# Performance work log

Hardware: AMD Instinct MI355X
Metric: run time of the kernel (lower is better)

The kernel has to match this reference:

```python
import jax, jax.numpy as jnp
import numpy as np

QW_MAX = 127  # 2**(8-1) - 1


def setup_inputs() -> dict:
    key = jax.random.key(0)
    k1, k2, k3, k4, k5 = jax.random.split(key, 5)
    B, Din, H, Dout = 4096, 1024, 4096, 1024
    x = jax.random.normal(k1, (B, Din), dtype=jnp.float32)
    # float master weights (already transposed, as in quantify_weights: weight.T)
    w1f = jax.random.normal(k2, (Din, H), dtype=jnp.float32) * 0.02
    b1f = jax.random.normal(k3, (H,), dtype=jnp.float32) * 0.02
    w2f = jax.random.normal(k4, (H, Dout), dtype=jnp.float32) * 0.02
    b2f = jax.random.normal(k5, (Dout,), dtype=jnp.float32) * 0.02
    return {"x": x, "w1f": w1f, "b1f": b1f, "w2f": w2f, "b2f": b2f}


def _quantify_pair(w, b):
    # joint max-abs scale over weight and bias (matches quantify(x, x2))
    max_v = jnp.maximum(jnp.max(jnp.abs(w)), jnp.max(jnp.abs(b)))
    scale = max_v / QW_MAX
    wq = jnp.round(w / scale).astype(jnp.int8)
    bq = jnp.round(b / scale).astype(jnp.int8)
    return wq, bq, scale


def _dot_product(q_a, q_b, scale_a, scale_b, target_scale):
    # int8 GEMM with int32 accumulation, then requantize to int16
    y0 = q_a.astype(jnp.int32) @ q_b.astype(jnp.int32)  # [M, N] int32
    scale = scale_a * scale_b / target_scale
    return jnp.round(y0 * scale).astype(jnp.int16)


def reference(x, w1f, b1f, w2f, b2f):
    # weight quantization (done once at init in torch, inlined here)
    w1, b1, s1 = _quantify_pair(w1f, b1f)
    w2, b2, s2 = _quantify_pair(w2f, b2f)
    # dynamic activation quantization
    x_scale = jnp.max(jnp.abs(x)) / QW_MAX
    x_q = jnp.round(x / x_scale).astype(jnp.int8)
    # layer 1: target_scale = s1, so effective multiplier is x_scale
    o1 = _dot_product(x_q, w1, x_scale, s1, s1) + b1.astype(jnp.int16)
    # layer 2: note torch passes scale_1 (not x_scale) here — faithful to source
    o2 = _dot_product(jnp.maximum(o1, 0), w2, s1, s2, s2) + b2.astype(jnp.int16)
    # dequantize
    return o2.astype(jnp.float32) * s2
```

## Files before the change

kernel.cpp:

```cpp
#include <hip/hip_runtime.h>
#include <stdint.h>

typedef int   i32x4 __attribute__((ext_vector_type(4)));
typedef float f32x4 __attribute__((ext_vector_type(4)));

#define WS_PART    0
#define WS_XQ      32768
#define WS_W1QT    (WS_XQ   + 4096*1024)
#define WS_W2QT    (WS_W1QT + 4096*1024)
#define WS_PS      (WS_W2QT + 4096*1024)
#define WS_PH      (WS_PS   + 4096*4096)

__device__ __forceinline__ void async16(const void* g, void* l) {
  __builtin_amdgcn_global_load_lds(
      (const __attribute__((address_space(1))) unsigned*)g,
      (__attribute__((address_space(3))) unsigned*)l, 16, 0, 0);
}

__device__ __forceinline__ float block_absmax(const float* __restrict__ p0, int n0,
                                              const float* __restrict__ p1, int n1,
                                              float* red, float* slot) {
  int tid = threadIdx.x, nt = blockDim.x;
  float m = 0.f;
  for (int i = tid; i < n0; i += nt) m = fmaxf(m, fabsf(p0[i]));
  if (p1) for (int i = tid; i < n1; i += nt) m = fmaxf(m, fabsf(p1[i]));
  for (int off = 32; off; off >>= 1) m = fmaxf(m, __shfl_down(m, off));
  if ((tid & 63) == 0) red[tid >> 6] = m;
  __syncthreads();
  if (tid == 0) {
    int nw = nt >> 6;
    float M = red[0];
    for (int w = 1; w < nw; w++) M = fmaxf(M, red[w]);
    *slot = M;
  }
  __syncthreads();
  return *slot;
}

__global__ void k_absmax3(const float* __restrict__ x, const float* __restrict__ w1,
                          const float* __restrict__ w2, float* __restrict__ part) {
  int seg = blockIdx.x >> 9;
  int b = blockIdx.x & 511;
  const float* p = (seg == 0) ? x : (seg == 1) ? w1 : w2;
  int i = b * 256 + threadIdx.x;
  float m = 0.f;
  #pragma unroll
  for (int it = 0; it < 8; it++) {
    f32x4 v = ((const f32x4*)p)[i + it * 131072];
    m = fmaxf(m, fmaxf(fmaxf(fabsf(v.x), fabsf(v.y)), fmaxf(fabsf(v.z), fabsf(v.w))));
  }
  for (int off = 32; off; off >>= 1) m = fmaxf(m, __shfl_down(m, off));
  __shared__ float red[4];
  if ((threadIdx.x & 63) == 0) red[threadIdx.x >> 6] = m;
  __syncthreads();
  if (threadIdx.x == 0)
    part[blockIdx.x] = fmaxf(fmaxf(red[0], red[1]), fmaxf(red[2], red[3]));
}

__device__ __forceinline__ void quantT_body(const float* __restrict__ w, float s,
                                            i32x4* __restrict__ out, int C, int tkbits,
                                            int b) {
  int L = b * 256 + threadIdx.x;
  int h_in = L & 127;
  int kb = (L >> 7) & 3;
  int tk = (L >> 9) & ((1 << tkbits) - 1);
  int hblk = L >> (9 + tkbits);
  int h = hblk * 128 + h_in;
  int k0 = (tk * 4 + kb) * 16;
  int wd[4];
  #pragma unroll
  for (int d = 0; d < 4; d++) {
    unsigned acc = 0;
    #pragma unroll
    for (int j = 0; j < 4; j++) {
      float v = w[(size_t)(k0 + d * 4 + j) * C + h];
      int q = (int)rintf(v / s) & 255;
      acc |= (unsigned)q << (8 * j);
    }
    wd[d] = (int)acc;
  }
  i32x4 o; o.x = wd[0]; o.y = wd[1]; o.z = wd[2]; o.w = wd[3];
  out[L] = o;
}

__global__ void k_prep(const float* __restrict__ x, const float* __restrict__ w1f,
                       const float* __restrict__ w2f, const float* __restrict__ b1f,
                       const float* __restrict__ b2f, const float* __restrict__ part,
                       i32x4* __restrict__ xq, i32x4* __restrict__ w1qt,
                       i32x4* __restrict__ w2qt) {
  __shared__ float red[4];
  __shared__ float slot;
  int seg = blockIdx.x >> 10;
  int b = blockIdx.x & 1023;
  if (seg == 0) {
    float s = block_absmax(part, 512, nullptr, 0, red, &slot) / 127.0f;
    int L = b * 256 + threadIdx.x;
    int m_in = L & 127, kb = (L >> 7) & 3, tk = (L >> 9) & 15, mblk = L >> 13;
    int m = mblk * 128 + m_in;
    int k0 = (tk * 4 + kb) * 16;
    const f32x4* px = (const f32x4*)(x + m * 1024 + k0);
    int wd[4];
    #pragma unroll
    for (int d = 0; d < 4; d++) {
      f32x4 v = px[d];
      int b0 = (int)rintf(v.x / s) & 255;
      int b1 = (int)rintf(v.y / s) & 255;
      int b2 = (int)rintf(v.z / s) & 255;
      int b3 = (int)rintf(v.w / s) & 255;
      wd[d] = b0 | (b1 << 8) | (b2 << 16) | (b3 << 24);
    }
    i32x4 o; o.x = wd[0]; o.y = wd[1]; o.z = wd[2]; o.w = wd[3];
    xq[L] = o;
  } else if (seg == 1) {
    float s = block_absmax(part + 512, 512, b1f, 4096, red, &slot) / 127.0f;
    quantT_body(w1f, s, w1qt, 4096, 4, b);
  } else {
    float s = block_absmax(part + 1024, 512, b2f, 1024, red, &slot) / 127.0f;
    quantT_body(w2f, s, w2qt, 1024, 6, b);
  }
}

__launch_bounds__(256, 4)
__global__ void k_gemm1(const i32x4* __restrict__ Aq, const i32x4* __restrict__ Bq,
                        const float* __restrict__ part, const float* __restrict__ b1f,
                        unsigned* __restrict__ plane_s, unsigned* __restrict__ plane_h) {
  __shared__ i32x4 As[2][512];
  __shared__ float red[4];
  __shared__ float slot;
  __shared__ int b1s[128];
  int tid = threadIdx.x;
  int bb = blockIdx.x;
  int hb = blockIdx.y;
  int lane = tid & 63, wid = tid >> 6;
  int wm = wid & 1, wn = wid >> 1;
  int g = lane >> 4, l15 = lane & 15;

  const i32x4* gA = Aq + (size_t)hb * 16 * 512;
  const i32x4* gB = Bq + (size_t)bb * 16 * 512;

  int abase = g * 128 + wm * 64 + l15;
  int bbase = g * 128 + wn * 64 + l15;

  async16(gA + tid, &As[0][tid]);
  async16(gA + tid + 256, &As[0][tid + 256]);
  i32x4 bnow[4];
  #pragma unroll
  for (int c = 0; c < 4; c++) bnow[c] = gB[bbase + c * 16];

  float sx  = block_absmax(part, 512, nullptr, 0, red, &slot) / 127.0f;
  float s1v = block_absmax(part + 512, 512, b1f, 4096, red, &slot) / 127.0f;
  float mult1 = sx * s1v / s1v;
  for (int i = tid; i < 128; i += 256)
    b1s[i] = (int)rintf(b1f[hb * 128 + i] / s1v);

  i32x4 acc[4][4];
  #pragma unroll
  for (int r = 0; r < 4; r++)
    #pragma unroll
    for (int c = 0; c < 4; c++) acc[r][c] = (i32x4)(0);

  for (int t = 0; t < 16; ++t) {
    int cur = t & 1;
    if (t + 1 < 16) {
      const i32x4* ga = gA + (t + 1) * 512;
      async16(ga + tid, &As[cur ^ 1][tid]);
      async16(ga + tid + 256, &As[cur ^ 1][tid + 256]);
    }
    i32x4 af[4];
    #pragma unroll
    for (int r = 0; r < 4; r++) af[r] = As[cur][abase + r * 16];
    #pragma unroll
    for (int r = 0; r < 4; r++)
      #pragma unroll
      for (int c = 0; c < 4; c++)
        acc[r][c] = __builtin_amdgcn_mfma_i32_16x16x64_i8(af[r], bnow[c], acc[r][c], 0, 0, 0);
    if (t + 1 < 16) {
      const i32x4* gb = gB + (t + 1) * 512;
      #pragma unroll
      for (int c = 0; c < 4; c++) bnow[c] = gb[bbase + c * 16];
    }
    __syncthreads();
  }

  int t2base = hb * 2 + wm;
  #pragma unroll
  for (int r = 0; r < 4; r++) {
    int hloc = wm * 64 + r * 16 + 4 * g;
    int bq0 = b1s[hloc], bq1 = b1s[hloc + 1], bq2 = b1s[hloc + 2], bq3 = b1s[hloc + 3];
    #pragma unroll
    for (int c = 0; c < 4; c++) {
      unsigned lo = 0, hi = 0;
      #pragma unroll
      for (int q = 0; q < 4; q++) {
        int y0 = acc[r][c][q];
        int bqv = (q == 0) ? bq0 : (q == 1) ? bq1 : (q == 2) ? bq2 : bq3;
        int o = (short)((int)rintf((float)y0 * mult1) + bqv);
        int a = o > 0 ? o : 0;
        int s8 = (int)(signed char)(a & 0xFF);
        int h8 = (a >> 8) + (s8 < 0 ? 1 : 0);
        lo |= (unsigned)(s8 & 0xFF) << (8 * q);
        hi |= (unsigned)(h8 & 0xFF) << (8 * q);
      }
      int m_in = wn * 64 + c * 16 + l15;
      unsigned idx = (((unsigned)(bb * 64 + t2base) * 512u + (unsigned)(r * 128 + m_in)) << 2) + g;
      plane_s[idx] = lo;
      plane_h[idx] = hi;
    }
  }
}

__launch_bounds__(512, 4)
__global__ void k_gemm2(const i32x4* __restrict__ Ps, const i32x4* __restrict__ Ph,
                        const i32x4* __restrict__ Bq, const float* __restrict__ part,
                        const float* __restrict__ b1f, const float* __restrict__ b2f,
                        float* __restrict__ out) {
  __shared__ i32x4 st[2048];
  __shared__ float red[8];
  __shared__ float slot;

  int tid = threadIdx.x;
  int L = blockIdx.x;
  int mb = ((L & 7) << 3) | ((L >> 3) & 7);
  int nb = L >> 6;
  int mblk = mb >> 1, half = mb & 1;
  int wid = tid >> 6, lane = tid & 63;
  int kh = wid >> 2, w2 = wid & 3;
  int wm = w2 & 1, wn = w2 >> 1;
  int g = lane >> 4, l15 = lane & 15;
  int t256 = tid & 255;
  int khbase = kh * 1024;
  int a_idx = (t256 >> 6) * 128 + half * 64 + (t256 & 63);
  int abase = g * 64 + wm * 32 + l15;
  int bbase = g * 128 + wn * 64 + l15;

  const i32x4* gS = Ps + (((size_t)mblk * 64 + kh * 32) << 9);
  const i32x4* gH = Ph + (((size_t)mblk * 64 + kh * 32) << 9);
  const i32x4* gB = Bq + (((size_t)nb * 64 + kh * 32) << 9);

  async16(gS + a_idx, &st[khbase + t256]);
  async16(gH + a_idx, &st[khbase + 256 + t256]);
  i32x4 bnow[4];
  #pragma unroll
  for (int c = 0; c < 4; c++) bnow[c] = gB[bbase + c * 16];

  float s1v = block_absmax(part + 512, 512, b1f, 4096, red, &slot) / 127.0f;
  float s2v = block_absmax(part + 1024, 512, b2f, 1024, red, &slot) / 127.0f;
  float mult2 = s1v * s2v / s2v;
  int bq[4];
  #pragma unroll
  for (int c = 0; c < 4; c++)
    bq[c] = (int)rintf(b2f[nb * 128 + wn * 64 + c * 16 + l15] / s2v);

  i32x4 accS[2][4], accH[2][4];
  #pragma unroll
  for (int r = 0; r < 2; r++)
    #pragma unroll
    for (int c = 0; c < 4; c++) { accS[r][c] = (i32x4)(0); accH[r][c] = (i32x4)(0); }

  for (int tt = 0; tt < 32; ++tt) {
    int cur = tt & 1;
    if (tt + 1 < 32) {
      const i32x4* pS = gS + ((size_t)(tt + 1) << 9);
      const i32x4* pH = gH + ((size_t)(tt + 1) << 9);
      int R1 = khbase + (cur ^ 1) * 512;
      async16(pS + a_idx, &st[R1 + t256]);
      async16(pH + a_idx, &st[R1 + 256 + t256]);
    }
    int R = khbase + cur * 512;
    i32x4 aS[2], aH[2];
    #pragma unroll
    for (int r = 0; r < 2; r++) {
      aS[r] = st[R + abase + r * 16];
      aH[r] = st[R + 256 + abase + r * 16];
    }
    #pragma unroll
    for (int r = 0; r < 2; r++)
      #pragma unroll
      for (int c = 0; c < 4; c++) {
        accS[r][c] = __builtin_amdgcn_mfma_i32_16x16x64_i8(aS[r], bnow[c], accS[r][c], 0, 0, 0);
        accH[r][c] = __builtin_amdgcn_mfma_i32_16x16x64_i8(aH[r], bnow[c], accH[r][c], 0, 0, 0);
      }
    if (tt + 1 < 32) {
      const i32x4* pB = gB + ((size_t)(tt + 1) << 9);
      #pragma unroll
      for (int c = 0; c < 4; c++) bnow[c] = pB[bbase + c * 16];
    }
    __syncthreads();
  }

  int* mg = (int*)st;
  if (kh == 1) {
    #pragma unroll
    for (int r = 0; r < 2; r++)
      #pragma unroll
      for (int c = 0; c < 4; c++)
        #pragma unroll
        for (int q = 0; q < 4; q++)
          mg[((r * 4 + c) * 4 + q) * 256 + t256] = accS[r][c][q] + accH[r][c][q] * 256;
  }
  __syncthreads();
  if (kh == 0) {
    #pragma unroll
    for (int r = 0; r < 2; r++) {
      int m0 = mb * 64 + wm * 32 + r * 16 + 4 * g;
      #pragma unroll
      for (int c = 0; c < 4; c++) {
        int n = nb * 128 + wn * 64 + c * 16 + l15;
        #pragma unroll
        for (int q = 0; q < 4; q++) {
          int y0 = accS[r][c][q] + accH[r][c][q] * 256
                 + mg[((r * 4 + c) * 4 + q) * 256 + t256];
          int o = (short)((int)rintf((float)y0 * mult2) + bq[c]);
          out[(size_t)(m0 + q) * 1024 + n] = (float)o * s2v;
        }
      }
    }
  }
}

extern "C" void kernel_launch(void* const* d_in, const int* in_sizes, int n_in,
                              void* d_out, int out_size, void* d_ws, size_t ws_size,
                              hipStream_t stream) {
  const float* x   = (const float*)d_in[0];
  const float* w1f = (const float*)d_in[1];
  const float* b1f = (const float*)d_in[2];
  const float* w2f = (const float*)d_in[3];
  const float* b2f = (const float*)d_in[4];
  float* out = (float*)d_out;

  char* ws = (char*)d_ws;
  float*  part    = (float*)(ws + WS_PART);
  i32x4*  xq      = (i32x4*)(ws + WS_XQ);
  i32x4*  w1qt    = (i32x4*)(ws + WS_W1QT);
  i32x4*  w2qt    = (i32x4*)(ws + WS_W2QT);
  unsigned* ps    = (unsigned*)(ws + WS_PS);
  unsigned* ph    = (unsigned*)(ws + WS_PH);

  k_absmax3<<<1536, 256, 0, stream>>>(x, w1f, w2f, part);
  k_prep<<<3072, 256, 0, stream>>>(x, w1f, w2f, b1f, b2f, part, xq, w1qt, w2qt);
  k_gemm1<<<dim3(32, 32), 256, 0, stream>>>(w1qt, xq, part, b1f, ps, ph);
  k_gemm2<<<512, 512, 0, stream>>>((const i32x4*)ps, (const i32x4*)ph, w2qt,
                                   part, b1f, b2f, out);
}
```

Baseline: 186.7 us.

## Drop LDS staging in both int8 GEMMs and load fragments directly from global

Both GEMM kernels stop staging A tiles through shared memory with async global-to-LDS copies and per-iteration barriers. Each wave now loads its MFMA fragments straight from global into registers, with a one-step register prefetch. The second GEMM uses 32-row tiles and twice as many blocks, and its split-K merge uses a smaller LDS buffer. This removes LDS traffic and barriers but gives up intra-block reuse of A tiles, so L2/global load traffic per MFMA rises.

```diff
diff --git a/kernel.cpp b/kernel.cpp
--- a/kernel.cpp
+++ b/kernel.cpp
@@ -10,12 +10,6 @@
 #define WS_W2QT    (WS_W1QT + 4096*1024)
 #define WS_PS      (WS_W2QT + 4096*1024)
 #define WS_PH      (WS_PS   + 4096*4096)
-
-__device__ __forceinline__ void async16(const void* g, void* l) {
-  __builtin_amdgcn_global_load_lds(
-      (const __attribute__((address_space(1))) unsigned*)g,
-      (__attribute__((address_space(3))) unsigned*)l, 16, 0, 0);
-}
 
 __device__ __forceinline__ float block_absmax(const float* __restrict__ p0, int n0,
                                               const float* __restrict__ p1, int n1,
@@ -124,7 +118,6 @@
 __global__ void k_gemm1(const i32x4* __restrict__ Aq, const i32x4* __restrict__ Bq,
                         const float* __restrict__ part, const float* __restrict__ b1f,
                         unsigned* __restrict__ plane_s, unsigned* __restrict__ plane_h) {
-  __shared__ i32x4 As[2][512];
   __shared__ float red[4];
   __shared__ float slot;
   __shared__ int b1s[128];
@@ -135,23 +128,20 @@
   int wm = wid & 1, wn = wid >> 1;
   int g = lane >> 4, l15 = lane & 15;
 
-  const i32x4* gA = Aq + (size_t)hb * 16 * 512;
-  const i32x4* gB = Bq + (size_t)bb * 16 * 512;
-
-  int abase = g * 128 + wm * 64 + l15;
-  int bbase = g * 128 + wn * 64 + l15;
-
-  async16(gA + tid, &As[0][tid]);
-  async16(gA + tid + 256, &As[0][tid + 256]);
-  i32x4 bnow[4];
-  #pragma unroll
-  for (int c = 0; c < 4; c++) bnow[c] = gB[bbase + c * 16];
+  const i32x4* gA = Aq + (size_t)hb * 16 * 512 + g * 128 + wm * 64 + l15;
+  const i32x4* gB = Bq + (size_t)bb * 16 * 512 + g * 128 + wn * 64 + l15;
+
+  i32x4 af[4], bf[4];
+  #pragma unroll
+  for (int r = 0; r < 4; r++) af[r] = gA[r * 16];
+  #pragma unroll
+  for (int c = 0; c < 4; c++) bf[c] = gB[c * 16];
 
   float sx  = block_absmax(part, 512, nullptr, 0, red, &slot) / 127.0f;
   float s1v = block_absmax(part + 512, 512, b1f, 4096, red, &slot) / 127.0f;
   float mult1 = sx * s1v / s1v;
-  for (int i = tid; i < 128; i += 256)
-    b1s[i] = (int)rintf(b1f[hb * 128 + i] / s1v);
+  if (tid < 128) b1s[tid] = (int)rintf(b1f[hb * 128 + tid] / s1v);
+  __syncthreads();
 
   i32x4 acc[4][4];
   #pragma unroll
@@ -160,26 +150,18 @@
     for (int c = 0; c < 4; c++) acc[r][c] = (i32x4)(0);
 
   for (int t = 0; t < 16; ++t) {
-    int cur = t & 1;
-    if (t + 1 < 16) {
-      const i32x4* ga = gA + (t + 1) * 512;
-      async16(ga + tid, &As[cur ^ 1][tid]);
-      async16(ga + tid + 256, &As[cur ^ 1][tid + 256]);
-    }
-    i32x4 af[4];
-    #pragma unroll
-    for (int r = 0; r < 4; r++) af[r] = As[cur][abase + r * 16];
-    #pragma unroll
-    for (int r = 0; r < 4; r++)
+    int tn = (t + 1 < 16) ? (t + 1) : 15;
+    const i32x4* gAn = gA + (size_t)tn * 512;
+    const i32x4* gBn = gB + (size_t)tn * 512;
+    #pragma unroll
+    for (int r = 0; r < 4; r++) {
       #pragma unroll
       for (int c = 0; c < 4; c++)
-        acc[r][c] = __builtin_amdgcn_mfma_i32_16x16x64_i8(af[r], bnow[c], acc[r][c], 0, 0, 0);
-    if (t + 1 < 16) {
-      const i32x4* gb = gB + (t + 1) * 512;
-      #pragma unroll
-      for (int c = 0; c < 4; c++) bnow[c] = gb[bbase + c * 16];
-    }
-    __syncthreads();
+        acc[r][c] = __builtin_amdgcn_mfma_i32_16x16x64_i8(af[r], bf[c], acc[r][c], 0, 0, 0);
+      af[r] = gAn[r * 16];
+    }
+    #pragma unroll
+    for (int c = 0; c < 4; c++) bf[c] = gBn[c * 16];
   }
 
   int t2base = hb * 2 + wm;
@@ -214,34 +196,28 @@
                         const i32x4* __restrict__ Bq, const float* __restrict__ part,
                         const float* __restrict__ b1f, const float* __restrict__ b2f,
                         float* __restrict__ out) {
-  __shared__ i32x4 st[2048];
   __shared__ float red[8];
   __shared__ float slot;
-
+  __shared__ int mg[32 * 128];
   int tid = threadIdx.x;
   int L = blockIdx.x;
-  int mb = ((L & 7) << 3) | ((L >> 3) & 7);
-  int nb = L >> 6;
-  int mblk = mb >> 1, half = mb & 1;
+  int mb = L & 127;
+  int nb = L >> 7;
+  int mblk = mb >> 2;
+  int m128 = (mb & 3) * 32;
   int wid = tid >> 6, lane = tid & 63;
   int kh = wid >> 2, w2 = wid & 3;
   int wm = w2 & 1, wn = w2 >> 1;
   int g = lane >> 4, l15 = lane & 15;
-  int t256 = tid & 255;
-  int khbase = kh * 1024;
-  int a_idx = (t256 >> 6) * 128 + half * 64 + (t256 & 63);
-  int abase = g * 64 + wm * 32 + l15;
-  int bbase = g * 128 + wn * 64 + l15;
-
-  const i32x4* gS = Ps + (((size_t)mblk * 64 + kh * 32) << 9);
-  const i32x4* gH = Ph + (((size_t)mblk * 64 + kh * 32) << 9);
-  const i32x4* gB = Bq + (((size_t)nb * 64 + kh * 32) << 9);
-
-  async16(gS + a_idx, &st[khbase + t256]);
-  async16(gH + a_idx, &st[khbase + 256 + t256]);
-  i32x4 bnow[4];
-  #pragma unroll
-  for (int c = 0; c < 4; c++) bnow[c] = gB[bbase + c * 16];
+
+  const i32x4* gS = Ps + (((size_t)mblk * 64 + kh * 32) << 9) + g * 128 + m128 + wm * 16 + l15;
+  const i32x4* gH = Ph + (((size_t)mblk * 64 + kh * 32) << 9) + g * 128 + m128 + wm * 16 + l15;
+  const i32x4* gB = Bq + (((size_t)nb * 64 + kh * 32) << 9) + g * 128 + wn * 64 + l15;
+
+  i32x4 aS = gS[0], aH = gH[0];
+  i32x4 bf[4];
+  #pragma unroll
+  for (int c = 0; c < 4; c++) bf[c] = gB[c * 16];
 
   float s1v = block_absmax(part + 512, 512, b1f, 4096, red, &slot) / 127.0f;
   float s2v = block_absmax(part + 1024, 512, b2f, 1024, red, &slot) / 127.0f;
@@ -251,68 +227,49 @@
   for (int c = 0; c < 4; c++)
     bq[c] = (int)rintf(b2f[nb * 128 + wn * 64 + c * 16 + l15] / s2v);
 
-  i32x4 accS[2][4], accH[2][4];
-  #pragma unroll
-  for (int r = 0; r < 2; r++)
-    #pragma unroll
-    for (int c = 0; c < 4; c++) { accS[r][c] = (i32x4)(0); accH[r][c] = (i32x4)(0); }
-
+  i32x4 accS[4], accH[4];
+  #pragma unroll
+  for (int c = 0; c < 4; c++) { accS[c] = (i32x4)(0); accH[c] = (i32x4)(0); }
+
+  #pragma unroll 2
   for (int tt = 0; tt < 32; ++tt) {
-    int cur = tt & 1;
-    if (tt + 1 < 32) {
-      const i32x4* pS = gS + ((size_t)(tt + 1) << 9);
-      const i32x4* pH = gH + ((size_t)(tt + 1) << 9);
-      int R1 = khbase + (cur ^ 1) * 512;
-      async16(pS + a_idx, &st[R1 + t256]);
-      async16(pH + a_idx, &st[R1 + 256 + t256]);
-    }
-    int R = khbase + cur * 512;
-    i32x4 aS[2], aH[2];
-    #pragma unroll
-    for (int r = 0; r < 2; r++) {
-      aS[r] = st[R + abase + r * 16];
-      aH[r] = st[R + 256 + abase + r * 16];
-    }
-    #pragma unroll
-    for (int r = 0; r < 2; r++)
+    int tn = (tt + 1 < 32) ? (tt + 1) : 31;
+    const i32x4* pS = gS + (size_t)tn * 512;
+    const i32x4* pH = gH + (size_t)tn * 512;
+    const i32x4* pB = gB + (size_t)tn * 512;
+    i32x4 aSn = pS[0], aHn = pH[0];
+    i32x4 bn[4];
+    #pragma unroll
+    for (int c = 0; c < 4; c++) bn[c] = pB[c * 16];
+    #pragma unroll
+    for (int c = 0; c < 4; c++) {
+      accS[c] = __builtin_amdgcn_mfma_i32_16x16x64_i8(aS, bf[c], accS[c], 0, 0, 0);
+      accH[c] = __builtin_amdgcn_mfma_i32_16x16x64_i8(aH, bf[c], accH[c], 0, 0, 0);
+    }
+    aS = aSn; aH = aHn;
+    #pragma unroll
+    for (int c = 0; c < 4; c++) bf[c] = bn[c];
+  }
+
+  if (kh == 1) {
+    #pragma unroll
+    for (int c = 0; c < 4; c++)
       #pragma unroll
-      for (int c = 0; c < 4; c++) {
-        accS[r][c] = __builtin_amdgcn_mfma_i32_16x16x64_i8(aS[r], bnow[c], accS[r][c], 0, 0, 0);
-        accH[r][c] = __builtin_amdgcn_mfma_i32_16x16x64_i8(aH[r], bnow[c], accH[r][c], 0, 0, 0);
-      }
-    if (tt + 1 < 32) {
-      const i32x4* pB = gB + ((size_t)(tt + 1) << 9);
+      for (int q = 0; q < 4; q++)
+        mg[(wm * 16 + 4 * g + q) * 128 + wn * 64 + c * 16 + l15] =
+            accS[c][q] + accH[c][q] * 256;
+  }
+  __syncthreads();
+  if (kh == 0) {
+    #pragma unroll
+    for (int c = 0; c < 4; c++) {
+      int n = nb * 128 + wn * 64 + c * 16 + l15;
       #pragma unroll
-      for (int c = 0; c < 4; c++) bnow[c] = pB[bbase + c * 16];
-    }
-    __syncthreads();
-  }
-
-  int* mg = (int*)st;
-  if (kh == 1) {
-    #pragma unroll
-    for (int r = 0; r < 2; r++)
-      #pragma unroll
-      for (int c = 0; c < 4; c++)
-        #pragma unroll
-        for (int q = 0; q < 4; q++)
-          mg[((r * 4 + c) * 4 + q) * 256 + t256] = accS[r][c][q] + accH[r][c][q] * 256;
-  }
-  __syncthreads();
-  if (kh == 0) {
-    #pragma unroll
-    for (int r = 0; r < 2; r++) {
-      int m0 = mb * 64 + wm * 32 + r * 16 + 4 * g;
-      #pragma unroll
-      for (int c = 0; c < 4; c++) {
-        int n = nb * 128 + wn * 64 + c * 16 + l15;
-        #pragma unroll
-        for (int q = 0; q < 4; q++) {
-          int y0 = accS[r][c][q] + accH[r][c][q] * 256
-                 + mg[((r * 4 + c) * 4 + q) * 256 + t256];
-          int o = (short)((int)rintf((float)y0 * mult2) + bq[c]);
-          out[(size_t)(m0 + q) * 1024 + n] = (float)o * s2v;
-        }
+      for (int q = 0; q < 4; q++) {
+        int rloc = wm * 16 + 4 * g + q;
+        int y0 = accS[c][q] + accH[c][q] * 256 + mg[rloc * 128 + wn * 64 + c * 16 + l15];
+        int o = (short)((int)rintf((float)y0 * mult2) + bq[c]);
+        out[(size_t)(mb * 32 + rloc) * 1024 + n] = (float)o * s2v;
       }
     }
   }
@@ -339,6 +296,6 @@
   k_absmax3<<<1536, 256, 0, stream>>>(x, w1f, w2f, part);
   k_prep<<<3072, 256, 0, stream>>>(x, w1f, w2f, b1f, b2f, part, xq, w1qt, w2qt);
   k_gemm1<<<dim3(32, 32), 256, 0, stream>>>(w1qt, xq, part, b1f, ps, ph);
-  k_gemm2<<<512, 512, 0, stream>>>((const i32x4*)ps, (const i32x4*)ph, w2qt,
-                                   part, b1f, b2f, out);
-}
+  k_gemm2<<<1024, 512, 0, stream>>>((const i32x4*)ps, (const i32x4*)ph, w2qt,
+                                    part, b1f, b2f, out);
+}
```

New measurement: 204.3 us. 1.09x slower.

## Triple-buffer A and B tiles in LDS for both GEMMs, drop split-K in gemm2

Applied to the files above, without the earlier changes.

Both int8 GEMM kernels now stage A and B tiles through LDS with a three-deep async buffer ring, prefetching two K-steps ahead. Before, B fragments were loaded straight from global memory into registers, which exposed that latency on every step. gemm2 also drops its two-wave-group split-K and the LDS merge at the end, running 256 threads over all 64 K-steps. This removes the reduction pass, but each block now does a longer serial K loop with fewer waves. LDS use grows and launch bounds go down to 3 blocks per CU, which may lower occupancy.

```diff
diff --git a/kernel.cpp b/kernel.cpp
--- a/kernel.cpp
+++ b/kernel.cpp
@@ -120,11 +120,12 @@
   }
 }
 
-__launch_bounds__(256, 4)
+__launch_bounds__(256, 3)
 __global__ void k_gemm1(const i32x4* __restrict__ Aq, const i32x4* __restrict__ Bq,
                         const float* __restrict__ part, const float* __restrict__ b1f,
                         unsigned* __restrict__ plane_s, unsigned* __restrict__ plane_h) {
-  __shared__ i32x4 As[2][512];
+  __shared__ i32x4 As[3][512];
+  __shared__ i32x4 Bs[3][512];
   __shared__ float red[4];
   __shared__ float slot;
   __shared__ int b1s[128];
@@ -141,17 +142,20 @@
   int abase = g * 128 + wm * 64 + l15;
   int bbase = g * 128 + wn * 64 + l15;
 
-  async16(gA + tid, &As[0][tid]);
-  async16(gA + tid + 256, &As[0][tid + 256]);
-  i32x4 bnow[4];
-  #pragma unroll
-  for (int c = 0; c < 4; c++) bnow[c] = gB[bbase + c * 16];
+  #pragma unroll
+  for (int p = 0; p < 2; p++) {
+    const i32x4* ga = gA + p * 512;
+    const i32x4* gb = gB + p * 512;
+    async16(ga + tid, &As[p][tid]);
+    async16(ga + tid + 256, &As[p][tid + 256]);
+    async16(gb + tid, &Bs[p][tid]);
+    async16(gb + tid + 256, &Bs[p][tid + 256]);
+  }
 
   float sx  = block_absmax(part, 512, nullptr, 0, red, &slot) / 127.0f;
   float s1v = block_absmax(part + 512, 512, b1f, 4096, red, &slot) / 127.0f;
   float mult1 = sx * s1v / s1v;
-  for (int i = tid; i < 128; i += 256)
-    b1s[i] = (int)rintf(b1f[hb * 128 + i] / s1v);
+  if (tid < 128) b1s[tid] = (int)rintf(b1f[hb * 128 + tid] / s1v);
 
   i32x4 acc[4][4];
   #pragma unroll
@@ -159,27 +163,29 @@
     #pragma unroll
     for (int c = 0; c < 4; c++) acc[r][c] = (i32x4)(0);
 
+  int cur = 0, wr = 2;
   for (int t = 0; t < 16; ++t) {
-    int cur = t & 1;
-    if (t + 1 < 16) {
-      const i32x4* ga = gA + (t + 1) * 512;
-      async16(ga + tid, &As[cur ^ 1][tid]);
-      async16(ga + tid + 256, &As[cur ^ 1][tid + 256]);
-    }
-    i32x4 af[4];
+    __syncthreads();
+    if (t + 2 < 16) {
+      const i32x4* ga = gA + (t + 2) * 512;
+      const i32x4* gb = gB + (t + 2) * 512;
+      async16(ga + tid, &As[wr][tid]);
+      async16(ga + tid + 256, &As[wr][tid + 256]);
+      async16(gb + tid, &Bs[wr][tid]);
+      async16(gb + tid + 256, &Bs[wr][tid + 256]);
+    }
+    i32x4 af[4], bf[4];
     #pragma unroll
     for (int r = 0; r < 4; r++) af[r] = As[cur][abase + r * 16];
+    #pragma unroll
+    for (int c = 0; c < 4; c++) bf[c] = Bs[cur][bbase + c * 16];
     #pragma unroll
     for (int r = 0; r < 4; r++)
       #pragma unroll
       for (int c = 0; c < 4; c++)
-        acc[r][c] = __builtin_amdgcn_mfma_i32_16x16x64_i8(af[r], bnow[c], acc[r][c], 0, 0, 0);
-    if (t + 1 < 16) {
-      const i32x4* gb = gB + (t + 1) * 512;
-      #pragma unroll
-      for (int c = 0; c < 4; c++) bnow[c] = gb[bbase + c * 16];
-    }
-    __syncthreads();
+        acc[r][c] = __builtin_amdgcn_mfma_i32_16x16x64_i8(af[r], bf[c], acc[r][c], 0, 0, 0);
+    cur = (cur == 2) ? 0 : cur + 1;
+    wr  = (wr  == 2) ? 0 : wr  + 1;
   }
 
   int t2base = hb * 2 + wm;
@@ -209,39 +215,39 @@
   }
 }
 
-__launch_bounds__(512, 4)
+__launch_bounds__(256, 3)
 __global__ void k_gemm2(const i32x4* __restrict__ Ps, const i32x4* __restrict__ Ph,
                         const i32x4* __restrict__ Bq, const float* __restrict__ part,
                         const float* __restrict__ b1f, const float* __restrict__ b2f,
                         float* __restrict__ out) {
-  __shared__ i32x4 st[2048];
-  __shared__ float red[8];
+  __shared__ i32x4 sS[3][256];
+  __shared__ i32x4 sH[3][256];
+  __shared__ i32x4 sB[3][512];
+  __shared__ float red[4];
   __shared__ float slot;
-
   int tid = threadIdx.x;
   int L = blockIdx.x;
   int mb = ((L & 7) << 3) | ((L >> 3) & 7);
   int nb = L >> 6;
   int mblk = mb >> 1, half = mb & 1;
-  int wid = tid >> 6, lane = tid & 63;
-  int kh = wid >> 2, w2 = wid & 3;
-  int wm = w2 & 1, wn = w2 >> 1;
+  int lane = tid & 63, wid = tid >> 6;
+  int wm = wid & 1, wn = wid >> 1;
   int g = lane >> 4, l15 = lane & 15;
-  int t256 = tid & 255;
-  int khbase = kh * 1024;
-  int a_idx = (t256 >> 6) * 128 + half * 64 + (t256 & 63);
+  int a_idx = (tid >> 6) * 128 + half * 64 + (tid & 63);
   int abase = g * 64 + wm * 32 + l15;
   int bbase = g * 128 + wn * 64 + l15;
 
-  const i32x4* gS = Ps + (((size_t)mblk * 64 + kh * 32) << 9);
-  const i32x4* gH = Ph + (((size_t)mblk * 64 + kh * 32) << 9);
-  const i32x4* gB = Bq + (((size_t)nb * 64 + kh * 32) << 9);
-
-  async16(gS + a_idx, &st[khbase + t256]);
-  async16(gH + a_idx, &st[khbase + 256 + t256]);
-  i32x4 bnow[4];
-  #pragma unroll
-  for (int c = 0; c < 4; c++) bnow[c] = gB[bbase + c * 16];
+  const i32x4* gS = Ps + ((size_t)mblk * 64 << 9);
+  const i32x4* gH = Ph + ((size_t)mblk * 64 << 9);
+  const i32x4* gB = Bq + ((size_t)nb * 64 << 9);
+
+  #pragma unroll
+  for (int p = 0; p < 2; p++) {
+    async16(gS + p * 512 + a_idx, &sS[p][tid]);
+    async16(gH + p * 512 + a_idx, &sH[p][tid]);
+    async16(gB + p * 512 + tid, &sB[p][tid]);
+    async16(gB + p * 512 + tid + 256, &sB[p][tid + 256]);
+  }
 
   float s1v = block_absmax(part + 512, 512, b1f, 4096, red, &slot) / 127.0f;
   float s2v = block_absmax(part + 1024, 512, b2f, 1024, red, &slot) / 127.0f;
@@ -257,62 +263,49 @@
     #pragma unroll
     for (int c = 0; c < 4; c++) { accS[r][c] = (i32x4)(0); accH[r][c] = (i32x4)(0); }
 
-  for (int tt = 0; tt < 32; ++tt) {
-    int cur = tt & 1;
-    if (tt + 1 < 32) {
-      const i32x4* pS = gS + ((size_t)(tt + 1) << 9);
-      const i32x4* pH = gH + ((size_t)(tt + 1) << 9);
-      int R1 = khbase + (cur ^ 1) * 512;
-      async16(pS + a_idx, &st[R1 + t256]);
-      async16(pH + a_idx, &st[R1 + 256 + t256]);
-    }
-    int R = khbase + cur * 512;
-    i32x4 aS[2], aH[2];
+  int cur = 0, wr = 2;
+  for (int t = 0; t < 64; ++t) {
+    __syncthreads();
+    if (t + 2 < 64) {
+      const i32x4* pS = gS + (size_t)(t + 2) * 512;
+      const i32x4* pH = gH + (size_t)(t + 2) * 512;
+      const i32x4* pB = gB + (size_t)(t + 2) * 512;
+      async16(pS + a_idx, &sS[wr][tid]);
+      async16(pH + a_idx, &sH[wr][tid]);
+      async16(pB + tid, &sB[wr][tid]);
+      async16(pB + tid + 256, &sB[wr][tid + 256]);
+    }
+    i32x4 aS[2], aH[2], bf[4];
     #pragma unroll
     for (int r = 0; r < 2; r++) {
-      aS[r] = st[R + abase + r * 16];
-      aH[r] = st[R + 256 + abase + r * 16];
-    }
+      aS[r] = sS[cur][abase + r * 16];
+      aH[r] = sH[cur][abase + r * 16];
+    }
+    #pragma unroll
+    for (int c = 0; c < 4; c++) bf[c] = sB[cur][bbase + c * 16];
     #pragma unroll
     for (int r = 0; r < 2; r++)
       #pragma unroll
       for (int c = 0; c < 4; c++) {
-        accS[r][c] = __builtin_amdgcn_mfma_i32_16x16x64_i8(aS[r], bnow[c], accS[r][c], 0, 0, 0);
-        accH[r][c] = __builtin_amdgcn_mfma_i32_16x16x64_i8(aH[r], bnow[c], accH[r][c], 0, 0, 0);
+        accS[r][c] = __builtin_amdgcn_mfma_i32_16x16x64_i8(aS[r], bf[c], accS[r][c], 0, 0, 0);
+        accH[r][c] = __builtin_amdgcn_mfma_i32_16x16x64_i8(aH[r], bf[c], accH[r][c], 0, 0, 0);
       }
-    if (tt + 1 < 32) {
-      const i32x4* pB = gB + ((size_t)(tt + 1) << 9);
+    cur = (cur == 2) ? 0 : cur + 1;
+    wr  = (wr  == 2) ? 0 : wr  + 1;
+  }
+
+  float s2 = s2v;
+  #pragma unroll
+  for (int r = 0; r < 2; r++) {
+    int m0 = mb * 64 + wm * 32 + r * 16 + 4 * g;
+    #pragma unroll
+    for (int c = 0; c < 4; c++) {
+      int n = nb * 128 + wn * 64 + c * 16 + l15;
       #pragma unroll
-      for (int c = 0; c < 4; c++) bnow[c] = pB[bbase + c * 16];
-    }
-    __syncthreads();
-  }
-
-  int* mg = (int*)st;
-  if (kh == 1) {
-    #pragma unroll
-    for (int r = 0; r < 2; r++)
-      #pragma unroll
-      for (int c = 0; c < 4; c++)
-        #pragma unroll
-        for (int q = 0; q < 4; q++)
-          mg[((r * 4 + c) * 4 + q) * 256 + t256] = accS[r][c][q] + accH[r][c][q] * 256;
-  }
-  __syncthreads();
-  if (kh == 0) {
-    #pragma unroll
-    for (int r = 0; r < 2; r++) {
-      int m0 = mb * 64 + wm * 32 + r * 16 + 4 * g;
-      #pragma unroll
-      for (int c = 0; c < 4; c++) {
-        int n = nb * 128 + wn * 64 + c * 16 + l15;
-        #pragma unroll
-        for (int q = 0; q < 4; q++) {
-          int y0 = accS[r][c][q] + accH[r][c][q] * 256
-                 + mg[((r * 4 + c) * 4 + q) * 256 + t256];
-          int o = (short)((int)rintf((float)y0 * mult2) + bq[c]);
-          out[(size_t)(m0 + q) * 1024 + n] = (float)o * s2v;
-        }
+      for (int q = 0; q < 4; q++) {
+        int y0 = accS[r][c][q] + accH[r][c][q] * 256;
+        int o = (short)((int)rintf((float)y0 * mult2) + bq[c]);
+        out[(size_t)(m0 + q) * 1024 + n] = (float)o * s2;
       }
     }
   }
@@ -339,6 +332,6 @@
   k_absmax3<<<1536, 256, 0, stream>>>(x, w1f, w2f, part);
   k_prep<<<3072, 256, 0, stream>>>(x, w1f, w2f, b1f, b2f, part, xq, w1qt, w2qt);
   k_gemm1<<<dim3(32, 32), 256, 0, stream>>>(w1qt, xq, part, b1f, ps, ph);
-  k_gemm2<<<512, 512, 0, stream>>>((const i32x4*)ps, (const i32x4*)ph, w2qt,
+  k_gemm2<<<512, 256, 0, stream>>>((const i32x4*)ps, (const i32x4*)ph, w2qt,
                                    part, b1f, b2f, out);
 }
```

Measured after the change: 192.7 us. 3.2% more time.

## Warp-specialize gemm2 with a dedicated loader wave and 4-stage LDS ring

Applied to the files above, without the earlier changes.

Restructures the second GEMM so that one wave only issues async global-to-LDS loads into a four-deep shared-memory ring, while four compute waves consume it through spin-wait ready/done flags. The K split across two wave groups and its LDS reduction go away, and B tiles now also come through LDS instead of per-wave global loads. The intent is to overlap memory and MFMA work without block-wide barriers. In exchange it relies on volatile spin loops and waitcnt encodings for correctness, and it has fewer compute waves per block.

```diff
diff --git a/kernel.cpp b/kernel.cpp
--- a/kernel.cpp
+++ b/kernel.cpp
@@ -10,6 +10,11 @@
 #define WS_W2QT    (WS_W1QT + 4096*1024)
 #define WS_PS      (WS_W2QT + 4096*1024)
 #define WS_PH      (WS_PS   + 4096*4096)
+
+#define WAIT_VM32  0x8F70
+#define WAIT_VM16  0x4F70
+#define WAIT_VM0   0x0F70
+#define WAIT_LGKM0 0xC07F
 
 __device__ __forceinline__ void async16(const void* g, void* l) {
   __builtin_amdgcn_global_load_lds(
@@ -209,97 +214,102 @@
   }
 }
 
-__launch_bounds__(512, 4)
+__launch_bounds__(320, 2)
 __global__ void k_gemm2(const i32x4* __restrict__ Ps, const i32x4* __restrict__ Ph,
                         const i32x4* __restrict__ Bq, const float* __restrict__ part,
                         const float* __restrict__ b1f, const float* __restrict__ b2f,
                         float* __restrict__ out) {
-  __shared__ i32x4 st[2048];
+  __shared__ i32x4 st[4][1024];
+  __shared__ int ready[4];
+  __shared__ int done[16];
   __shared__ float red[8];
   __shared__ float slot;
+  volatile int* vready = (volatile int*)ready;
+  volatile int* vdone  = (volatile int*)done;
 
   int tid = threadIdx.x;
   int L = blockIdx.x;
   int mb = ((L & 7) << 3) | ((L >> 3) & 7);
   int nb = L >> 6;
   int mblk = mb >> 1, half = mb & 1;
-  int wid = tid >> 6, lane = tid & 63;
-  int kh = wid >> 2, w2 = wid & 3;
-  int wm = w2 & 1, wn = w2 >> 1;
+  int lane = tid & 63, wid = tid >> 6;
+  int wm = wid & 1, wn = wid >> 1;
   int g = lane >> 4, l15 = lane & 15;
-  int t256 = tid & 255;
-  int khbase = kh * 1024;
-  int a_idx = (t256 >> 6) * 128 + half * 64 + (t256 & 63);
   int abase = g * 64 + wm * 32 + l15;
-  int bbase = g * 128 + wn * 64 + l15;
-
-  const i32x4* gS = Ps + (((size_t)mblk * 64 + kh * 32) << 9);
-  const i32x4* gH = Ph + (((size_t)mblk * 64 + kh * 32) << 9);
-  const i32x4* gB = Bq + (((size_t)nb * 64 + kh * 32) << 9);
-
-  async16(gS + a_idx, &st[khbase + t256]);
-  async16(gH + a_idx, &st[khbase + 256 + t256]);
-  i32x4 bnow[4];
-  #pragma unroll
-  for (int c = 0; c < 4; c++) bnow[c] = gB[bbase + c * 16];
-
+  int bbase = 512 + g * 128 + wn * 64 + l15;
+
+  const i32x4* gS = Ps + ((size_t)mblk * 64 << 9);
+  const i32x4* gH = Ph + ((size_t)mblk * 64 << 9);
+  const i32x4* gB = Bq + ((size_t)nb * 64 << 9);
+
+  if (tid < 4) ready[tid] = -1;
+  if (tid < 16) done[tid] = -1;
   float s1v = block_absmax(part + 512, 512, b1f, 4096, red, &slot) / 127.0f;
   float s2v = block_absmax(part + 1024, 512, b2f, 1024, red, &slot) / 127.0f;
   float mult2 = s1v * s2v / s2v;
-  int bq[4];
-  #pragma unroll
-  for (int c = 0; c < 4; c++)
-    bq[c] = (int)rintf(b2f[nb * 128 + wn * 64 + c * 16 + l15] / s2v);
-
-  i32x4 accS[2][4], accH[2][4];
-  #pragma unroll
-  for (int r = 0; r < 2; r++)
-    #pragma unroll
-    for (int c = 0; c < 4; c++) { accS[r][c] = (i32x4)(0); accH[r][c] = (i32x4)(0); }
-
-  for (int tt = 0; tt < 32; ++tt) {
-    int cur = tt & 1;
-    if (tt + 1 < 32) {
-      const i32x4* pS = gS + ((size_t)(tt + 1) << 9);
-      const i32x4* pH = gH + ((size_t)(tt + 1) << 9);
-      int R1 = khbase + (cur ^ 1) * 512;
-      async16(pS + a_idx, &st[R1 + t256]);
-      async16(pH + a_idx, &st[R1 + 256 + t256]);
-    }
-    int R = khbase + cur * 512;
-    i32x4 aS[2], aH[2];
-    #pragma unroll
-    for (int r = 0; r < 2; r++) {
-      aS[r] = st[R + abase + r * 16];
-      aH[r] = st[R + 256 + abase + r * 16];
-    }
+
+  if (wid == 4) {
+    for (int p = 0; p < 64; ++p) {
+      int buf = p & 3;
+      while (vdone[buf * 4 + 0] < p - 4 || vdone[buf * 4 + 1] < p - 4 ||
+             vdone[buf * 4 + 2] < p - 4 || vdone[buf * 4 + 3] < p - 4) { }
+      __asm__ __volatile__("" ::: "memory");
+      const i32x4* pS = gS + ((size_t)p << 9);
+      const i32x4* pH = gH + ((size_t)p << 9);
+      const i32x4* pB = gB + ((size_t)p << 9);
+      #pragma unroll
+      for (int j = 0; j < 4; j++)
+        async16(pS + (j * 128 + half * 64 + lane), &st[buf][j * 64 + lane]);
+      #pragma unroll
+      for (int j = 0; j < 4; j++)
+        async16(pH + (j * 128 + half * 64 + lane), &st[buf][256 + j * 64 + lane]);
+      #pragma unroll
+      for (int j = 0; j < 8; j++)
+        async16(pB + (j * 64 + lane), &st[buf][512 + j * 64 + lane]);
+      if (p >= 2) {
+        __builtin_amdgcn_s_waitcnt(WAIT_VM32);
+        vready[(p - 2) & 3] = p - 2;
+      }
+    }
+    __builtin_amdgcn_s_waitcnt(WAIT_VM16);
+    vready[62 & 3] = 62;
+    __builtin_amdgcn_s_waitcnt(WAIT_VM0);
+    vready[63 & 3] = 63;
+  } else {
+    i32x4 accS[2][4], accH[2][4];
     #pragma unroll
     for (int r = 0; r < 2; r++)
       #pragma unroll
-      for (int c = 0; c < 4; c++) {
-        accS[r][c] = __builtin_amdgcn_mfma_i32_16x16x64_i8(aS[r], bnow[c], accS[r][c], 0, 0, 0);
-        accH[r][c] = __builtin_amdgcn_mfma_i32_16x16x64_i8(aH[r], bnow[c], accH[r][c], 0, 0, 0);
+      for (int c = 0; c < 4; c++) { accS[r][c] = (i32x4)(0); accH[r][c] = (i32x4)(0); }
+    int bq[4];
+    #pragma unroll
+    for (int c = 0; c < 4; c++)
+      bq[c] = (int)rintf(b2f[nb * 128 + wn * 64 + c * 16 + l15] / s2v);
+
+    for (int t = 0; t < 64; ++t) {
+      int buf = t & 3;
+      while (vready[buf] < t) { }
+      __asm__ __volatile__("" ::: "memory");
+      i32x4 aS[2], aH[2], bf[4];
+      #pragma unroll
+      for (int r = 0; r < 2; r++) {
+        aS[r] = st[buf][abase + r * 16];
+        aH[r] = st[buf][256 + abase + r * 16];
       }
-    if (tt + 1 < 32) {
-      const i32x4* pB = gB + ((size_t)(tt + 1) << 9);
-      #pragma unroll
-      for (int c = 0; c < 4; c++) bnow[c] = pB[bbase + c * 16];
-    }
-    __syncthreads();
-  }
-
-  int* mg = (int*)st;
-  if (kh == 1) {
-    #pragma unroll
-    for (int r = 0; r < 2; r++)
-      #pragma unroll
-      for (int c = 0; c < 4; c++)
+      #pragma unroll
+      for (int c = 0; c < 4; c++) bf[c] = st[buf][bbase + c * 16];
+      #pragma unroll
+      for (int r = 0; r < 2; r++)
         #pragma unroll
-        for (int q = 0; q < 4; q++)
-          mg[((r * 4 + c) * 4 + q) * 256 + t256] = accS[r][c][q] + accH[r][c][q] * 256;
-  }
-  __syncthreads();
-  if (kh == 0) {
+        for (int c = 0; c < 4; c++) {
+          accS[r][c] = __builtin_amdgcn_mfma_i32_16x16x64_i8(aS[r], bf[c], accS[r][c], 0, 0, 0);
+          accH[r][c] = __builtin_amdgcn_mfma_i32_16x16x64_i8(aH[r], bf[c], accH[r][c], 0, 0, 0);
+        }
+      __builtin_amdgcn_s_waitcnt(WAIT_LGKM0);
+      __asm__ __volatile__("" ::: "memory");
+      vdone[buf * 4 + wid] = t;
+    }
+
     #pragma unroll
     for (int r = 0; r < 2; r++) {
       int m0 = mb * 64 + wm * 32 + r * 16 + 4 * g;
@@ -308,8 +318,7 @@
         int n = nb * 128 + wn * 64 + c * 16 + l15;
         #pragma unroll
         for (int q = 0; q < 4; q++) {
-          int y0 = accS[r][c][q] + accH[r][c][q] * 256
-                 + mg[((r * 4 + c) * 4 + q) * 256 + t256];
+          int y0 = accS[r][c][q] + accH[r][c][q] * 256;
           int o = (short)((int)rintf((float)y0 * mult2) + bq[c]);
           out[(size_t)(m0 + q) * 1024 + n] = (float)o * s2v;
         }
@@ -339,6 +348,6 @@
   k_absmax3<<<1536, 256, 0, stream>>>(x, w1f, w2f, part);
   k_prep<<<3072, 256, 0, stream>>>(x, w1f, w2f, b1f, b2f, part, xq, w1qt, w2qt);
   k_gemm1<<<dim3(32, 32), 256, 0, stream>>>(w1qt, xq, part, b1f, ps, ph);
-  k_gemm2<<<512, 512, 0, stream>>>((const i32x4*)ps, (const i32x4*)ph, w2qt,
+  k_gemm2<<<512, 320, 0, stream>>>((const i32x4*)ps, (const i32x4*)ph, w2qt,
                                    part, b1f, b2f, out);
 }
```

Measured after the change: 246.8 us. 32.1% more time.
